# Kernel optimization log

Hardware: AMD Instinct MI355X
Metric: run time of the kernel (lower is better)

The kernel has to match this reference:

```python
import jax, jax.numpy as jnp
import numpy as np

N_NODES = 100000


def _gcn_conv(x, edge_index, W, b, num_nodes):
    """PyG GCNConv: x' = D^{-1/2} (A + I) D^{-1/2} (x W) + b."""
    xl = x @ W  # [N, H]
    loop = jnp.arange(num_nodes)
    row = jnp.concatenate([edge_index[0], loop])  # source
    col = jnp.concatenate([edge_index[1], loop])  # target
    deg = jax.ops.segment_sum(jnp.ones_like(col, dtype=xl.dtype), col,
                              num_segments=num_nodes)
    dinv = jnp.where(deg > 0, jax.lax.rsqrt(deg), 0.0)
    norm = dinv[row] * dinv[col]  # [E + N]
    msgs = xl[row] * norm[:, None]  # gather + scale
    out = jax.ops.segment_sum(msgs, col, num_segments=num_nodes)
    return out + b


def setup_inputs() -> dict:
    key = jax.random.key(0)
    ks = jax.random.split(key, 6)
    N, E, D, H, O = N_NODES, 1600000, 128, 64, 1
    x = jax.random.normal(ks[0], (N, D), dtype=jnp.float32)
    edge_index = jax.random.randint(ks[1], (2, E), 0, N, dtype=jnp.int64)
    W1 = jax.random.normal(ks[2], (D, H), dtype=jnp.float32) / np.sqrt(D)
    b1 = jnp.zeros((H,), dtype=jnp.float32)
    W2 = jax.random.normal(ks[3], (H, H), dtype=jnp.float32) / np.sqrt(H)
    b2 = jnp.zeros((H,), dtype=jnp.float32)
    Wfc = jax.random.normal(ks[4], (H, O), dtype=jnp.float32) / np.sqrt(H)
    bfc = jnp.zeros((O,), dtype=jnp.float32)
    return {"x": x, "edge_index": edge_index, "W1": W1, "b1": b1,
            "W2": W2, "b2": b2, "Wfc": Wfc, "bfc": bfc}


def reference(x, edge_index, W1, b1, W2, b2, Wfc, bfc):
    N = x.shape[0]
    h = jax.nn.relu(_gcn_conv(x, edge_index, W1, b1, N))
    h = jax.nn.relu(_gcn_conv(h, edge_index, W2, b2, N))
    return jax.nn.sigmoid(h @ Wfc + bfc)  # [N, 1]
```

## Files before the change

### kernel.cpp

```cpp
#include <hip/hip_runtime.h>
#include <math.h>


typedef __attribute__((ext_vector_type(8))) short bf16x8;
typedef __attribute__((ext_vector_type(4))) float f32x4;
typedef __attribute__((ext_vector_type(2))) float f32x2;

#define CHUNKS 1024

__device__ __forceinline__ unsigned short f2bf(float f) {
    unsigned u = __float_as_uint(f);
    u += 0x7FFFu + ((u >> 16) & 1u);
    return (unsigned short)(u >> 16);
}
__device__ __forceinline__ unsigned packbf(float a, float b) {
    return (unsigned)f2bf(a) | ((unsigned)f2bf(b) << 16);
}
__device__ __forceinline__ void upadd2(uint4 g, f32x2* a) {
    a[0] += (f32x2){__uint_as_float(g.x << 16), __uint_as_float(g.x & 0xFFFF0000u)};
    a[1] += (f32x2){__uint_as_float(g.y << 16), __uint_as_float(g.y & 0xFFFF0000u)};
    a[2] += (f32x2){__uint_as_float(g.z << 16), __uint_as_float(g.z & 0xFFFF0000u)};
    a[3] += (f32x2){__uint_as_float(g.w << 16), __uint_as_float(g.w & 0xFFFF0000u)};
}
__device__ __forceinline__ unsigned char f2fp8(float f) {
    return (unsigned char)(__builtin_amdgcn_cvt_pk_fp8_f32(f, f, 0u, false) & 0xFFu);
}
__device__ __forceinline__ void fp8add(uint2 g, f32x2* a) {
    a[0] += __builtin_amdgcn_cvt_pk_f32_fp8((int)g.x, false);
    a[1] += __builtin_amdgcn_cvt_pk_f32_fp8((int)g.x, true);
    a[2] += __builtin_amdgcn_cvt_pk_f32_fp8((int)g.y, false);
    a[3] += __builtin_amdgcn_cvt_pk_f32_fp8((int)g.y, true);
}

__global__ __launch_bounds__(256) void k_hist(const int* __restrict__ col, int E,
                                              int NBUK, int CH,
                                              int* __restrict__ hist_g) {
    __shared__ int h[256];
    for (int i = threadIdx.x; i < NBUK; i += 256) h[i] = 0;
    __syncthreads();
    int base = blockIdx.x * CH, hi = min(base + CH, E);
    for (int e = base + (int)threadIdx.x; e < hi; e += 256)
        atomicAdd(&h[col[e] >> 9], 1);
    __syncthreads();
    for (int i = threadIdx.x; i < NBUK; i += 256)
        hist_g[blockIdx.x * NBUK + i] = h[i];
}

__global__ __launch_bounds__(256) void k_colscan(const int* __restrict__ hist_g, int NBUK,
                                                 int* __restrict__ histOff,
                                                 int* __restrict__ bucketTotal) {
    __shared__ int s[256];
    const int b = blockIdx.x, t = threadIdx.x;
    int v[4], sum = 0;
#pragma unroll
    for (int j = 0; j < 4; ++j) {
        v[j] = hist_g[(t * 4 + j) * NBUK + b];
        sum += v[j];
    }
    s[t] = sum;
    __syncthreads();
    for (int off = 1; off < 256; off <<= 1) {
        int u = (t >= off) ? s[t - off] : 0;
        __syncthreads();
        s[t] += u;
        __syncthreads();
    }
    int run = s[t] - sum;
#pragma unroll
    for (int j = 0; j < 4; ++j) {
        histOff[b * CHUNKS + t * 4 + j] = run;
        run += v[j];
    }
    if (t == 255) bucketTotal[b] = run;
}

__global__ __launch_bounds__(256) void k_scan_tot(const int* __restrict__ bucketTotal,
                                                  int NBUK, int E, int N,
                                                  int* __restrict__ bucketBase,
                                                  int* __restrict__ row_off) {
    __shared__ int s[256];
    int t = threadIdx.x;
    int v = (t < NBUK) ? bucketTotal[t] : 0;
    s[t] = v;
    __syncthreads();
    for (int off = 1; off < 256; off <<= 1) {
        int u = (t >= off) ? s[t - off] : 0;
        __syncthreads();
        s[t] += u;
        __syncthreads();
    }
    if (t < NBUK) bucketBase[t] = s[t] - v;
    if (t == 0) row_off[N] = E;
}

__global__ __launch_bounds__(256) void k_scatter(const int* __restrict__ row,
                                                 const int* __restrict__ col, int E,
                                                 int NBUK, int CH,
                                                 const int* __restrict__ bucketBase,
                                                 const int* __restrict__ histOff,
                                                 unsigned* __restrict__ ebuf) {
    __shared__ int cur[256];
    for (int i = threadIdx.x; i < NBUK; i += 256)
        cur[i] = bucketBase[i] + histOff[i * CHUNKS + blockIdx.x];
    __syncthreads();
    int base = blockIdx.x * CH, hi = min(base + CH, E);
    for (int e = base + (int)threadIdx.x; e < hi; e += 256) {
        int d = col[e], src = row[e];
        int b = d >> 9;
        int pos = atomicAdd(&cur[b], 1);
        ebuf[pos] = ((unsigned)(d & 511) << 17) | (unsigned)src;
    }
}

__global__ __launch_bounds__(512) void k_bucket(const unsigned* __restrict__ ebuf,
                                                const int* __restrict__ bucketBase,
                                                const int* __restrict__ bucketTotal,
                                                int N,
                                                int* __restrict__ row_off,
                                                float* __restrict__ dinv,
                                                int* __restrict__ csr_src) {
    __shared__ int hc[512], of[512];
    const int bid = blockIdx.x, t = threadIdx.x;
    const int base = bucketBase[bid];
    const int cnt  = bucketTotal[bid];
    hc[t] = 0;
    __syncthreads();
    for (int i = t; i < cnt; i += 512)
        atomicAdd(&hc[ebuf[base + i] >> 17], 1);
    __syncthreads();
    int v = hc[t];
    of[t] = v;
    __syncthreads();
    for (int off = 1; off < 512; off <<= 1) {
        int u = (t >= off) ? of[t - off] : 0;
        __syncthreads();
        of[t] += u;
        __syncthreads();
    }
    int excl = of[t] - v;
    int node = bid * 512 + t;
    if (node < N) {
        row_off[node] = base + excl;
        dinv[node] = rsqrtf((float)(v + 1));
    }
    of[t] = excl;
    __syncthreads();
    for (int i = t; i < cnt; i += 512) {
        unsigned e = ebuf[base + i];
        int dl = (int)(e >> 17), src = (int)(e & 0x1FFFFu);
        int pos = atomicAdd(&of[dl], 1);
        csr_src[base + pos] = src;
    }
}

template <int K>
__global__ __launch_bounds__(256) void k_gemm_mfma(const float* __restrict__ xf,
                                                   const float* __restrict__ W,
                                                   const float* __restrict__ dinv,
                                                   unsigned char* __restrict__ out,
                                                   int N) {
    constexpr int KS = K + 8;
    __shared__ short sX[64 * KS];
    __shared__ short sW[64 * KS];
    const int tid = threadIdx.x;
    const int wv = tid >> 6, lane = tid & 63;
    const int q = lane >> 4, m = lane & 15;
    const int nb = blockIdx.x * 64;

    for (int i = tid; i < K * 64; i += 256) {
        int k = i >> 6, c = i & 63;
        sW[c * KS + k] = (short)f2bf(W[i]);
    }
    for (int i = tid; i < 64 * (K / 8); i += 256) {
        int r = i / (K / 8), c8 = (i % (K / 8)) * 8;
        int node = nb + r;
        uint4 v = make_uint4(0u, 0u, 0u, 0u);
        if (node < N) {
            float4 lo = *(const float4*)(xf + (size_t)node * K + c8);
            float4 hi = *(const float4*)(xf + (size_t)node * K + c8 + 4);
            v.x = packbf(lo.x, lo.y);
            v.y = packbf(lo.z, lo.w);
            v.z = packbf(hi.x, hi.y);
            v.w = packbf(hi.z, hi.w);
        }
        *(uint4*)(&sX[r * KS + c8]) = v;
    }
    __syncthreads();

    f32x4 acc[4] = {};
    const short* aRow = &sX[(wv * 16 + m) * KS + q * 8];
#pragma unroll
    for (int k0 = 0; k0 < K; k0 += 32) {
        bf16x8 a = *(const bf16x8*)(aRow + k0);
#pragma unroll
        for (int ft = 0; ft < 4; ++ft) {
            bf16x8 b = *(const bf16x8*)(&sW[(ft * 16 + m) * KS + k0 + q * 8]);
            acc[ft] = __builtin_amdgcn_mfma_f32_16x16x32_bf16(a, b, acc[ft], 0, 0, 0);
        }
    }
#pragma unroll
    for (int r = 0; r < 4; ++r) {
        int node = nb + wv * 16 + q * 4 + r;
        if (node < N) {
            float di = dinv[node];
#pragma unroll
            for (int ft = 0; ft < 4; ++ft)
                out[(size_t)node * 64 + ft * 16 + m] = f2fp8(acc[ft][r] * di);
        }
    }
}

__global__ __launch_bounds__(256) void k_agg_g2(const unsigned char* __restrict__ xl,
                                                const int* __restrict__ row_off,
                                                const int* __restrict__ csr_src,
                                                const float* __restrict__ dinv,
                                                const float* __restrict__ bias,
                                                const float* __restrict__ W2,
                                                unsigned char* __restrict__ out, int N) {
    constexpr int KS = 72;
    __shared__ short sH[4 * 16 * KS];
    __shared__ short sW2[64 * KS];
    const int tid = threadIdx.x;
    const int wv = tid >> 6, lane = tid & 63;
    const int s = lane >> 3, o = lane & 7;
    const int q = lane >> 4, m = lane & 15;

    for (int i = tid; i < 64 * 64; i += 256) {
        int k = i >> 6, n = i & 63;
        sW2[n * KS + k] = (short)f2bf(W2[i]);
    }
    short* myH = &sH[wv * 16 * KS];
    for (int i = lane; i < 8 * KS / 4; i += 64)
        ((unsigned long long*)(myH + 8 * KS))[i] = 0ull;
    __syncthreads();

    const int base8 = (blockIdx.x * 4 + wv) * 8;
    int node = base8 + s;
    const bool active = node < N;
    node = min(node, N - 1);
    const int beg = row_off[node];
    const int deg = row_off[node + 1] - beg;
    const int cnt = active ? deg + 1 : 0;
    int mx = cnt;
    mx = max(mx, __shfl_xor(mx, 8, 64));
    mx = max(mx, __shfl_xor(mx, 16, 64));
    mx = max(mx, __shfl_xor(mx, 32, 64));
    const char* xlb = (const char*)xl;
    const unsigned loff = (unsigned)(o << 3);
    f32x2 acc0[4] = {}, acc1[4] = {};
    int idx[4];
#pragma unroll
    for (int j = 0; j < 4; ++j) idx[j] = (j < deg) ? csr_src[beg + j] : node;
    for (int it = 0; it < mx; it += 4) {
        int c[4];
        bool v[4];
#pragma unroll
        for (int j = 0; j < 4; ++j) {
            c[j] = idx[j];
            v[j] = (it + j) < cnt;
            idx[j] = (it + 4 + j < deg) ? csr_src[beg + it + 4 + j] : node;
        }
        uint2 g0 = *(const uint2*)(xlb + (((unsigned)c[0] << 6) | loff));
        uint2 g1 = *(const uint2*)(xlb + (((unsigned)c[1] << 6) | loff));
        uint2 g2 = *(const uint2*)(xlb + (((unsigned)c[2] << 6) | loff));
        uint2 g3 = *(const uint2*)(xlb + (((unsigned)c[3] << 6) | loff));
        if (!v[0]) g0 = make_uint2(0u, 0u);
        if (!v[1]) g1 = make_uint2(0u, 0u);
        if (!v[2]) g2 = make_uint2(0u, 0u);
        if (!v[3]) g3 = make_uint2(0u, 0u);
        fp8add(g0, acc0);
        fp8add(g1, acc1);
        fp8add(g2, acc0);
        fp8add(g3, acc1);
    }
#pragma unroll
    for (int j = 0; j < 4; ++j) acc0[j] += acc1[j];
    {
        float di = dinv[node];
        float4 blo = *(const float4*)(bias + o * 8);
        float4 bhi = *(const float4*)(bias + o * 8 + 4);
        uint4 h;
        h.x = packbf(fmaxf(acc0[0].x * di + blo.x, 0.f), fmaxf(acc0[0].y * di + blo.y, 0.f));
        h.y = packbf(fmaxf(acc0[1].x * di + blo.z, 0.f), fmaxf(acc0[1].y * di + blo.w, 0.f));
        h.z = packbf(fmaxf(acc0[2].x * di + bhi.x, 0.f), fmaxf(acc0[2].y * di + bhi.y, 0.f));
        h.w = packbf(fmaxf(acc0[3].x * di + bhi.z, 0.f), fmaxf(acc0[3].y * di + bhi.w, 0.f));
        *(uint4*)(myH + s * KS + o * 8) = h;
    }
    f32x4 accm[4] = {};
#pragma unroll
    for (int k0 = 0; k0 < 64; k0 += 32) {
        bf16x8 a = *(const bf16x8*)(myH + m * KS + q * 8 + k0);
#pragma unroll
        for (int ft = 0; ft < 4; ++ft) {
            bf16x8 b = *(const bf16x8*)(&sW2[(ft * 16 + m) * KS + k0 + q * 8]);
            accm[ft] = __builtin_amdgcn_mfma_f32_16x16x32_bf16(a, b, accm[ft], 0, 0, 0);
        }
    }
    if (q < 2) {
#pragma unroll
        for (int r = 0; r < 4; ++r) {
            int node2 = base8 + q * 4 + r;
            if (node2 < N) {
                float di2 = dinv[node2];
#pragma unroll
                for (int ft = 0; ft < 4; ++ft)
                    out[(size_t)node2 * 64 + ft * 16 + m] = f2fp8(accm[ft][r] * di2);
            }
        }
    }
}

__global__ __launch_bounds__(256) void k_agg_fc(const unsigned char* __restrict__ xl,
                                                const int* __restrict__ row_off,
                                                const int* __restrict__ csr_src,
                                                const float* __restrict__ dinv,
                                                const float* __restrict__ bias,
                                                const float* __restrict__ Wfc,
                                                const float* __restrict__ bfc,
                                                float* __restrict__ out, int N) {
    const int wave = threadIdx.x >> 6, lane = threadIdx.x & 63;
    const int s = lane >> 3, o = lane & 7;
    int node = (blockIdx.x * 4 + wave) * 8 + s;
    const bool active = node < N;
    node = min(node, N - 1);
    const int beg = row_off[node];
    const int deg = row_off[node + 1] - beg;
    const int cnt = active ? deg + 1 : 0;
    int mx = cnt;
    mx = max(mx, __shfl_xor(mx, 8, 64));
    mx = max(mx, __shfl_xor(mx, 16, 64));
    mx = max(mx, __shfl_xor(mx, 32, 64));
    const char* xlb = (const char*)xl;
    const unsigned loff = (unsigned)(o << 3);
    f32x2 acc0[4] = {}, acc1[4] = {};
    int idx[4];
#pragma unroll
    for (int j = 0; j < 4; ++j) idx[j] = (j < deg) ? csr_src[beg + j] : node;
    for (int it = 0; it < mx; it += 4) {
        int c[4];
        bool v[4];
#pragma unroll
        for (int j = 0; j < 4; ++j) {
            c[j] = idx[j];
            v[j] = (it + j) < cnt;
            idx[j] = (it + 4 + j < deg) ? csr_src[beg + it + 4 + j] : node;
        }
        uint2 g0 = *(const uint2*)(xlb + (((unsigned)c[0] << 6) | loff));
        uint2 g1 = *(const uint2*)(xlb + (((unsigned)c[1] << 6) | loff));
        uint2 g2 = *(const uint2*)(xlb + (((unsigned)c[2] << 6) | loff));
        uint2 g3 = *(const uint2*)(xlb + (((unsigned)c[3] << 6) | loff));
        if (!v[0]) g0 = make_uint2(0u, 0u);
        if (!v[1]) g1 = make_uint2(0u, 0u);
        if (!v[2]) g2 = make_uint2(0u, 0u);
        if (!v[3]) g3 = make_uint2(0u, 0u);
        fp8add(g0, acc0);
        fp8add(g1, acc1);
        fp8add(g2, acc0);
        fp8add(g3, acc1);
    }
#pragma unroll
    for (int j = 0; j < 4; ++j) acc0[j] += acc1[j];
    const float di = dinv[node];
    float4 blo = *(const float4*)(bias + o * 8);
    float4 bhi = *(const float4*)(bias + o * 8 + 4);
    float4 wlo = *(const float4*)(Wfc + o * 8);
    float4 whi = *(const float4*)(Wfc + o * 8 + 4);
    float v = 0.f;
    v += fmaxf(acc0[0].x * di + blo.x, 0.f) * wlo.x;
    v += fmaxf(acc0[0].y * di + blo.y, 0.f) * wlo.y;
    v += fmaxf(acc0[1].x * di + blo.z, 0.f) * wlo.z;
    v += fmaxf(acc0[1].y * di + blo.w, 0.f) * wlo.w;
    v += fmaxf(acc0[2].x * di + bhi.x, 0.f) * whi.x;
    v += fmaxf(acc0[2].y * di + bhi.y, 0.f) * whi.y;
    v += fmaxf(acc0[3].x * di + bhi.z, 0.f) * whi.z;
    v += fmaxf(acc0[3].y * di + bhi.w, 0.f) * whi.w;
    v += __shfl_xor(v, 1, 64);
    v += __shfl_xor(v, 2, 64);
    v += __shfl_xor(v, 4, 64);
    if (active && o == 0) out[node] = 1.f / (1.f + expf(-(v + bfc[0])));
}

extern "C" void kernel_launch(void* const* d_in, const int* in_sizes, int n_in,
                              void* d_out, int out_size, void* d_ws, size_t ws_size,
                              hipStream_t stream) {
    const float* x   = (const float*)d_in[0];
    const int*   ei  = (const int*)d_in[1];
    const float* W1  = (const float*)d_in[2];
    const float* b1  = (const float*)d_in[3];
    const float* W2  = (const float*)d_in[4];
    const float* b2  = (const float*)d_in[5];
    const float* Wfc = (const float*)d_in[6];
    const float* bfc = (const float*)d_in[7];
    float* out = (float*)d_out;

    const int H = in_sizes[3];
    const int D = in_sizes[2] / H;
    const int N = in_sizes[0] / D;
    const int E = in_sizes[1] / 2;
    const int* row = ei;
    const int* col = ei + E;
    const int NBUK = (N + 511) >> 9;
    const int CH   = (E + CHUNKS - 1) / CHUNKS;

    char* p = (char*)d_ws;
    auto carve = [&](size_t bytes) {
        char* r = p;
        p += (bytes + 255) & ~(size_t)255;
        return (void*)r;
    };
    int*            hist_g      = (int*)carve((size_t)CHUNKS * 256 * 4);
    int*            histOff     = (int*)carve((size_t)256 * CHUNKS * 4);
    int*            bucketTotal = (int*)carve((size_t)256 * 4);
    int*            bucketBase  = (int*)carve((size_t)256 * 4);
    unsigned*       ebuf        = (unsigned*)carve((size_t)E * 4);
    int*            csr_src     = (int*)carve((size_t)E * 4);
    int*            row_off     = (int*)carve((size_t)(N + 1) * 4);
    float*          dinv        = (float*)carve((size_t)N * 4);
    unsigned char*  bufXL8      = (unsigned char*)carve((size_t)N * 64);
    unsigned char*  bufXL2      = (unsigned char*)carve((size_t)N * 64);
    (void)ws_size;

    const int TB = 256;
    k_hist<<<CHUNKS, TB, 0, stream>>>(col, E, NBUK, CH, hist_g);
    k_colscan<<<NBUK, TB, 0, stream>>>(hist_g, NBUK, histOff, bucketTotal);
    k_scan_tot<<<1, TB, 0, stream>>>(bucketTotal, NBUK, E, N, bucketBase, row_off);
    k_scatter<<<CHUNKS, TB, 0, stream>>>(row, col, E, NBUK, CH, bucketBase, histOff, ebuf);
    k_bucket<<<NBUK, 512, 0, stream>>>(ebuf, bucketBase, bucketTotal, N,
                                       row_off, dinv, csr_src);

    int gemmGrid = (N + 63) / 64;
    int aggGrid  = (N + 31) / 32;
    k_gemm_mfma<128><<<gemmGrid, TB, 0, stream>>>(x, W1, dinv, bufXL8, N);
    k_agg_g2<<<aggGrid, TB, 0, stream>>>(bufXL8, row_off, csr_src, dinv, b1, W2, bufXL2, N);
    k_agg_fc<<<aggGrid, TB, 0, stream>>>(bufXL2, row_off, csr_src, dinv, b2, Wfc, bfc, out, N);
}
```

Baseline: 203.9 us.

## Build CSR with global per-node atomics instead of two-pass bucket sort

Replaces the two-level bucket sort (per-chunk histograms, column scan, bucket scatter, in-bucket sort) with a direct CSR build. Degrees are counted with global atomics per node, scanned per block and then fixed up, and edges are filled using a global per-node cursor atomic. This drops the intermediate edge buffer and the big histogram arrays, but it relies on 1.6M global atomics scattered across 100k counters twice, and the fill writes land at random positions. Edge order within each row also becomes nondeterministic.

```diff
diff --git a/kernel.cpp b/kernel.cpp
--- a/kernel.cpp
+++ b/kernel.cpp
@@ -15,12 +15,6 @@
 }
 __device__ __forceinline__ unsigned packbf(float a, float b) {
     return (unsigned)f2bf(a) | ((unsigned)f2bf(b) << 16);
-}
-__device__ __forceinline__ void upadd2(uint4 g, f32x2* a) {
-    a[0] += (f32x2){__uint_as_float(g.x << 16), __uint_as_float(g.x & 0xFFFF0000u)};
-    a[1] += (f32x2){__uint_as_float(g.y << 16), __uint_as_float(g.y & 0xFFFF0000u)};
-    a[2] += (f32x2){__uint_as_float(g.z << 16), __uint_as_float(g.z & 0xFFFF0000u)};
-    a[3] += (f32x2){__uint_as_float(g.w << 16), __uint_as_float(g.w & 0xFFFF0000u)};
 }
 __device__ __forceinline__ unsigned char f2fp8(float f) {
     return (unsigned char)(__builtin_amdgcn_cvt_pk_fp8_f32(f, f, 0u, false) & 0xFFu);
@@ -32,46 +26,41 @@
     a[3] += __builtin_amdgcn_cvt_pk_f32_fp8((int)g.y, true);
 }
 
-__global__ __launch_bounds__(256) void k_hist(const int* __restrict__ col, int E,
-                                              int NBUK, int CH,
-                                              int* __restrict__ hist_g) {
-    __shared__ int h[256];
-    for (int i = threadIdx.x; i < NBUK; i += 256) h[i] = 0;
-    __syncthreads();
+__global__ __launch_bounds__(256) void k_zero(int* __restrict__ deg, int N) {
+    int i = blockIdx.x * 256 + threadIdx.x;
+    if (i < N) deg[i] = 0;
+}
+
+__global__ __launch_bounds__(256) void k_deg(const int* __restrict__ col, int E, int CH,
+                                             int* __restrict__ deg) {
     int base = blockIdx.x * CH, hi = min(base + CH, E);
     for (int e = base + (int)threadIdx.x; e < hi; e += 256)
-        atomicAdd(&h[col[e] >> 9], 1);
+        atomicAdd(&deg[col[e]], 1);
+}
+
+__global__ __launch_bounds__(512) void k_part(const int* __restrict__ deg, int N,
+                                              int* __restrict__ row_off,
+                                              float* __restrict__ dinv,
+                                              int* __restrict__ cur,
+                                              int* __restrict__ bucketTotal) {
+    __shared__ int s[512];
+    const int b = blockIdx.x, t = threadIdx.x;
+    const int node = b * 512 + t;
+    int d = (node < N) ? deg[node] : 0;
+    s[t] = d;
     __syncthreads();
-    for (int i = threadIdx.x; i < NBUK; i += 256)
-        hist_g[blockIdx.x * NBUK + i] = h[i];
-}
-
-__global__ __launch_bounds__(256) void k_colscan(const int* __restrict__ hist_g, int NBUK,
-                                                 int* __restrict__ histOff,
-                                                 int* __restrict__ bucketTotal) {
-    __shared__ int s[256];
-    const int b = blockIdx.x, t = threadIdx.x;
-    int v[4], sum = 0;
-#pragma unroll
-    for (int j = 0; j < 4; ++j) {
-        v[j] = hist_g[(t * 4 + j) * NBUK + b];
-        sum += v[j];
-    }
-    s[t] = sum;
-    __syncthreads();
-    for (int off = 1; off < 256; off <<= 1) {
+    for (int off = 1; off < 512; off <<= 1) {
         int u = (t >= off) ? s[t - off] : 0;
         __syncthreads();
         s[t] += u;
         __syncthreads();
     }
-    int run = s[t] - sum;
-#pragma unroll
-    for (int j = 0; j < 4; ++j) {
-        histOff[b * CHUNKS + t * 4 + j] = run;
-        run += v[j];
-    }
-    if (t == 255) bucketTotal[b] = run;
+    if (node < N) {
+        row_off[node] = s[t] - d;
+        dinv[node] = rsqrtf((float)(d + 1));
+        cur[node] = 0;
+    }
+    if (t == 511) bucketTotal[b] = s[t];
 }
 
 __global__ __launch_bounds__(256) void k_scan_tot(const int* __restrict__ bucketTotal,
@@ -93,63 +82,22 @@
     if (t == 0) row_off[N] = E;
 }
 
-__global__ __launch_bounds__(256) void k_scatter(const int* __restrict__ row,
-                                                 const int* __restrict__ col, int E,
-                                                 int NBUK, int CH,
-                                                 const int* __restrict__ bucketBase,
-                                                 const int* __restrict__ histOff,
-                                                 unsigned* __restrict__ ebuf) {
-    __shared__ int cur[256];
-    for (int i = threadIdx.x; i < NBUK; i += 256)
-        cur[i] = bucketBase[i] + histOff[i * CHUNKS + blockIdx.x];
-    __syncthreads();
+__global__ __launch_bounds__(512) void k_fix(int N, const int* __restrict__ bucketBase,
+                                             int* __restrict__ row_off) {
+    int node = blockIdx.x * 512 + (int)threadIdx.x;
+    if (node < N) row_off[node] += bucketBase[blockIdx.x];
+}
+
+__global__ __launch_bounds__(256) void k_fill(const int* __restrict__ row,
+                                              const int* __restrict__ col, int E, int CH,
+                                              const int* __restrict__ row_off,
+                                              int* __restrict__ cur,
+                                              int* __restrict__ csr_src) {
     int base = blockIdx.x * CH, hi = min(base + CH, E);
     for (int e = base + (int)threadIdx.x; e < hi; e += 256) {
-        int d = col[e], src = row[e];
-        int b = d >> 9;
-        int pos = atomicAdd(&cur[b], 1);
-        ebuf[pos] = ((unsigned)(d & 511) << 17) | (unsigned)src;
-    }
-}
-
-__global__ __launch_bounds__(512) void k_bucket(const unsigned* __restrict__ ebuf,
-                                                const int* __restrict__ bucketBase,
-                                                const int* __restrict__ bucketTotal,
-                                                int N,
-                                                int* __restrict__ row_off,
-                                                float* __restrict__ dinv,
-                                                int* __restrict__ csr_src) {
-    __shared__ int hc[512], of[512];
-    const int bid = blockIdx.x, t = threadIdx.x;
-    const int base = bucketBase[bid];
-    const int cnt  = bucketTotal[bid];
-    hc[t] = 0;
-    __syncthreads();
-    for (int i = t; i < cnt; i += 512)
-        atomicAdd(&hc[ebuf[base + i] >> 17], 1);
-    __syncthreads();
-    int v = hc[t];
-    of[t] = v;
-    __syncthreads();
-    for (int off = 1; off < 512; off <<= 1) {
-        int u = (t >= off) ? of[t - off] : 0;
-        __syncthreads();
-        of[t] += u;
-        __syncthreads();
-    }
-    int excl = of[t] - v;
-    int node = bid * 512 + t;
-    if (node < N) {
-        row_off[node] = base + excl;
-        dinv[node] = rsqrtf((float)(v + 1));
-    }
-    of[t] = excl;
-    __syncthreads();
-    for (int i = t; i < cnt; i += 512) {
-        unsigned e = ebuf[base + i];
-        int dl = (int)(e >> 17), src = (int)(e & 0x1FFFFu);
-        int pos = atomicAdd(&of[dl], 1);
-        csr_src[base + pos] = src;
+        int d = col[e];
+        int pos = atomicAdd(&cur[d], 1);
+        csr_src[row_off[d] + pos] = row[e];
     }
 }
 
@@ -408,11 +356,10 @@
         p += (bytes + 255) & ~(size_t)255;
         return (void*)r;
     };
-    int*            hist_g      = (int*)carve((size_t)CHUNKS * 256 * 4);
-    int*            histOff     = (int*)carve((size_t)256 * CHUNKS * 4);
+    int*            deg         = (int*)carve((size_t)N * 4);
+    int*            cur         = (int*)carve((size_t)N * 4);
     int*            bucketTotal = (int*)carve((size_t)256 * 4);
     int*            bucketBase  = (int*)carve((size_t)256 * 4);
-    unsigned*       ebuf        = (unsigned*)carve((size_t)E * 4);
     int*            csr_src     = (int*)carve((size_t)E * 4);
     int*            row_off     = (int*)carve((size_t)(N + 1) * 4);
     float*          dinv        = (float*)carve((size_t)N * 4);
@@ -421,12 +368,12 @@
     (void)ws_size;
 
     const int TB = 256;
-    k_hist<<<CHUNKS, TB, 0, stream>>>(col, E, NBUK, CH, hist_g);
-    k_colscan<<<NBUK, TB, 0, stream>>>(hist_g, NBUK, histOff, bucketTotal);
+    k_zero<<<(N + 255) / 256, TB, 0, stream>>>(deg, N);
+    k_deg<<<CHUNKS, TB, 0, stream>>>(col, E, CH, deg);
+    k_part<<<NBUK, 512, 0, stream>>>(deg, N, row_off, dinv, cur, bucketTotal);
     k_scan_tot<<<1, TB, 0, stream>>>(bucketTotal, NBUK, E, N, bucketBase, row_off);
-    k_scatter<<<CHUNKS, TB, 0, stream>>>(row, col, E, NBUK, CH, bucketBase, histOff, ebuf);
-    k_bucket<<<NBUK, 512, 0, stream>>>(ebuf, bucketBase, bucketTotal, N,
-                                       row_off, dinv, csr_src);
+    k_fix<<<NBUK, 512, 0, stream>>>(N, bucketBase, row_off);
+    k_fill<<<CHUNKS, TB, 0, stream>>>(row, col, E, CH, row_off, cur, csr_src);
 
     int gemmGrid = (N + 63) / 64;
     int aggGrid  = (N + 31) / 32;
```

Result: slower. 315.8 us (+54.9%).
